# Kernel optimization log

Hardware: AMD Instinct MI355X
Metric: run time of the kernel (lower is better)

The kernel has to match this reference:

```python
import jax, jax.numpy as jnp
import numpy as np


def setup_inputs() -> dict:
    key = jax.random.key(0)
    k_x, k_wxh, k_whh, k_fcw, k_fcb = jax.random.split(key, 5)
    B, T, I, H = 256, 512, 64, 512
    x = jax.random.normal(k_x, (B, T, I), dtype=jnp.float32)
    W_xh = jax.random.normal(k_wxh, (I, H), dtype=jnp.float32) * 0.01
    W_hh = jax.random.normal(k_whh, (H, H), dtype=jnp.float32) * 0.01
    b = jnp.zeros((H,), dtype=jnp.float32)
    # nn.Linear(H, 1): weight (1, H), bias (1); init ~ U(-1/sqrt(H), 1/sqrt(H))
    lim = 1.0 / np.sqrt(H)
    fc_w = jax.random.uniform(k_fcw, (1, H), dtype=jnp.float32, minval=-lim, maxval=lim)
    fc_b = jax.random.uniform(k_fcb, (1,), dtype=jnp.float32, minval=-lim, maxval=lim)
    return {"x": x, "W_xh": W_xh, "W_hh": W_hh, "b": b, "fc_w": fc_w, "fc_b": fc_b}


def reference(x, W_xh, W_hh, b, fc_w, fc_b):
    B, T, I = x.shape
    H = W_hh.shape[0]
    # Precompute input projections for all timesteps in one big matmul: (B,T,H)
    xh = jnp.einsum('bti,ih->bth', x, W_xh) + b
    h0 = jnp.zeros((B, H), dtype=x.dtype)

    def step(h, xh_t):
        h_new = jnp.tanh(xh_t + h @ W_hh)
        return h_new, None

    h_final, _ = jax.lax.scan(step, h0, jnp.swapaxes(xh, 0, 1))  # scan over T
    return h_final @ fc_w.T + fc_b  # (B, 1)
```

## Files before the change

### kernel.cpp

```cpp
#include <hip/hip_runtime.h>


#define BATCH    256
#define TSTEPS   512
#define IDIM     64
#define HDIM     512
#define NTH      512

typedef _Float16 half2_t __attribute__((ext_vector_type(2)));
typedef _Float16 half8_t __attribute__((ext_vector_type(8)));

union H8U {
    half8_t v;
    half2_t p[4];
    uint4   u4;
};

__device__ __forceinline__ float fdot2(half2_t a, half2_t b, float c) {
#if __has_builtin(__builtin_amdgcn_fdot2)
    return __builtin_amdgcn_fdot2(a, b, c, false);
#else
    return c + (float)a[0] * (float)b[0] + (float)a[1] * (float)b[1];
#endif
}

__device__ __forceinline__ float fast_tanh(float x) {
    float e = __builtin_amdgcn_exp2f(x * 2.88539008177792681472f);
    return 1.0f - 2.0f * __builtin_amdgcn_rcpf(e + 1.0f);
}

__device__ __forceinline__ float quad_sum(float x) {
    union { float f; int i; } a, b;
    a.f = x;
    b.i = __builtin_amdgcn_update_dpp(0, a.i, 0xB1, 0xF, 0xF, true);
    a.f += b.f;
    b.i = __builtin_amdgcn_update_dpp(0, a.i, 0x4E, 0xF, 0xF, true);
    a.f += b.f;
    return a.f;
}

#define XH_ROWS 16
__global__ __launch_bounds__(NTH, 4)
void xh_gemm(const float* __restrict__ x, const float* __restrict__ Wxh,
             const float* __restrict__ bias, _Float16* __restrict__ xh)
{
    const int j = threadIdx.x;
    const size_t r0 = (size_t)blockIdx.x * XH_ROWS;
    float wcol[IDIM];
#pragma unroll
    for (int i = 0; i < IDIM; ++i) wcol[i] = Wxh[(size_t)i * HDIM + j];
    const float bj = bias[j];
#pragma unroll
    for (int r = 0; r < XH_ROWS; ++r) {
        const float* xr = x + (r0 + r) * IDIM;
        float acc = bj;
#pragma unroll
        for (int i = 0; i < IDIM; ++i) acc += xr[i] * wcol[i];
        xh[(r0 + r) * HDIM + j] = (_Float16)acc;
    }
}

#define K4_RP      48
#define K4_NW      (4 * K4_RP)
#define K4_STR     17
#define K4_W_BYTES (NTH * K4_STR * 16)
#define K4_HB_OFF   K4_W_BYTES
#define K4_HB_STRIDE 1152
#define K4_RED_OFF  (K4_HB_OFF + 2 * K4_HB_STRIDE)
#define K4_SMEM_BYTES (K4_RED_OFF + 64)

__global__ __attribute__((amdgpu_flat_work_group_size(NTH, NTH), amdgpu_waves_per_eu(2, 2)))
void rnn_k4s(const _Float16* __restrict__ xh,
             const float* __restrict__ Whh,
             const float* __restrict__ fcw,
             const float* __restrict__ fcb,
             float* __restrict__ out)
{
    extern __shared__ char smem[];
    uint4* ldsW = reinterpret_cast<uint4*>(smem);
    float* red  = reinterpret_cast<float*>(smem + K4_RED_OFF);

    const int tid   = threadIdx.x;
    const int q     = tid & 3;
    const int c     = tid >> 2;
    const int j0    = 4 * c;
    const int kbase = 128 * q;
    const int b     = blockIdx.x;

    half2_t wr[K4_NW];
    uint4*  myW = ldsW + tid * K4_STR;
#pragma unroll
    for (int p = 0; p < K4_RP; ++p) {
        const float4 f0 = *reinterpret_cast<const float4*>(Whh + (size_t)(kbase + 2 * p) * HDIM + j0);
        const float4 f1 = *reinterpret_cast<const float4*>(Whh + (size_t)(kbase + 2 * p + 1) * HDIM + j0);
        half2_t w;
        w[0] = (_Float16)f0.x; w[1] = (_Float16)f1.x; wr[4 * p + 0] = w;
        w[0] = (_Float16)f0.y; w[1] = (_Float16)f1.y; wr[4 * p + 1] = w;
        w[0] = (_Float16)f0.z; w[1] = (_Float16)f1.z; wr[4 * p + 2] = w;
        w[0] = (_Float16)f0.w; w[1] = (_Float16)f1.w; wr[4 * p + 3] = w;
    }
#pragma unroll
    for (int cc = 0; cc < 4; ++cc) {
        H8U t0, t1, t2, t3;
#pragma unroll
        for (int e = 0; e < 4; ++e) {
            const int k = kbase + 96 + 8 * cc + 2 * e;
            const float4 f0 = *reinterpret_cast<const float4*>(Whh + (size_t)k * HDIM + j0);
            const float4 f1 = *reinterpret_cast<const float4*>(Whh + (size_t)(k + 1) * HDIM + j0);
            half2_t w;
            w[0] = (_Float16)f0.x; w[1] = (_Float16)f1.x; t0.p[e] = w;
            w[0] = (_Float16)f0.y; w[1] = (_Float16)f1.y; t1.p[e] = w;
            w[0] = (_Float16)f0.z; w[1] = (_Float16)f1.z; t2.p[e] = w;
            w[0] = (_Float16)f0.w; w[1] = (_Float16)f1.w; t3.p[e] = w;
        }
        myW[cc]      = t0.u4;
        myW[4 + cc]  = t1.u4;
        myW[8 + cc]  = t2.u4;
        myW[12 + cc] = t3.u4;
    }

    const char* hb0c = smem + K4_HB_OFF + 288 * q;
    const char* hb1c = hb0c + K4_HB_STRIDE;
    const int   jw   = j0 + q;
    const int   wbyte = 2 * jw + 32 * (jw >> 7);
    _Float16* wp0 = reinterpret_cast<_Float16*>(smem + K4_HB_OFF + wbyte);
    _Float16* wp1 = reinterpret_cast<_Float16*>(smem + K4_HB_OFF + K4_HB_STRIDE + wbyte);

    const float fcwj = fcw[jw];
    const _Float16* xhp = xh + (size_t)b * TSTEPS * HDIM + jw;

    if (tid < 144) {
        uint4 z; z.x = z.y = z.z = z.w = 0u;
        reinterpret_cast<uint4*>(smem + K4_HB_OFF)[tid] = z;
    }
    __syncthreads();

    float hlast = 0.f;
#pragma unroll 1
    for (int t = 0; t < TSTEPS; ++t) {
        const _Float16* hb = reinterpret_cast<const _Float16*>((t & 1) ? hb1c : hb0c);
        const float xv = (float)*xhp;
        xhp += HDIM;

        float a0 = 0.f, b0 = 0.f, a1 = 0.f, b1 = 0.f;
        float a2 = 0.f, b2 = 0.f, a3 = 0.f, b3 = 0.f;
#pragma unroll
        for (int i = 0; i < 12; ++i) {
            H8U u; u.v = *reinterpret_cast<const half8_t*>(hb + 8 * i);
            a0 = fdot2(u.p[0], wr[16*i +  0], a0);
            a1 = fdot2(u.p[0], wr[16*i +  1], a1);
            a2 = fdot2(u.p[0], wr[16*i +  2], a2);
            a3 = fdot2(u.p[0], wr[16*i +  3], a3);
            b0 = fdot2(u.p[1], wr[16*i +  4], b0);
            b1 = fdot2(u.p[1], wr[16*i +  5], b1);
            b2 = fdot2(u.p[1], wr[16*i +  6], b2);
            b3 = fdot2(u.p[1], wr[16*i +  7], b3);
            a0 = fdot2(u.p[2], wr[16*i +  8], a0);
            a1 = fdot2(u.p[2], wr[16*i +  9], a1);
            a2 = fdot2(u.p[2], wr[16*i + 10], a2);
            a3 = fdot2(u.p[2], wr[16*i + 11], a3);
            b0 = fdot2(u.p[3], wr[16*i + 12], b0);
            b1 = fdot2(u.p[3], wr[16*i + 13], b1);
            b2 = fdot2(u.p[3], wr[16*i + 14], b2);
            b3 = fdot2(u.p[3], wr[16*i + 15], b3);
        }
#pragma unroll
        for (int cc = 0; cc < 4; ++cc) {
            H8U u; u.v = *reinterpret_cast<const half8_t*>(hb + 8 * (12 + cc));
            H8U w0; w0.u4 = myW[cc];
            H8U w1; w1.u4 = myW[4 + cc];
            H8U w2; w2.u4 = myW[8 + cc];
            H8U w3; w3.u4 = myW[12 + cc];
            a0 = fdot2(u.p[0], w0.p[0], a0); b0 = fdot2(u.p[1], w0.p[1], b0);
            a0 = fdot2(u.p[2], w0.p[2], a0); b0 = fdot2(u.p[3], w0.p[3], b0);
            a1 = fdot2(u.p[0], w1.p[0], a1); b1 = fdot2(u.p[1], w1.p[1], b1);
            a1 = fdot2(u.p[2], w1.p[2], a1); b1 = fdot2(u.p[3], w1.p[3], b1);
            a2 = fdot2(u.p[0], w2.p[0], a2); b2 = fdot2(u.p[1], w2.p[1], b2);
            a2 = fdot2(u.p[2], w2.p[2], a2); b2 = fdot2(u.p[3], w2.p[3], b2);
            a3 = fdot2(u.p[0], w3.p[0], a3); b3 = fdot2(u.p[1], w3.p[1], b3);
            a3 = fdot2(u.p[2], w3.p[2], a3); b3 = fdot2(u.p[3], w3.p[3], b3);
        }

        const float s0 = quad_sum(a0 + b0);
        const float s1 = quad_sum(a1 + b1);
        const float s2 = quad_sum(a2 + b2);
        const float s3 = quad_sum(a3 + b3);

        const float sq = (q & 2) ? ((q & 1) ? s3 : s2) : ((q & 1) ? s1 : s0);
        const float h  = fast_tanh(sq + xv);
        *((t & 1) ? wp0 : wp1) = (_Float16)h;
        hlast = h;
        __syncthreads();
    }

    float partial = hlast * fcwj;
#pragma unroll
    for (int off = 32; off >= 1; off >>= 1)
        partial += __shfl_down(partial, off, 64);
    if ((tid & 63) == 0) red[tid >> 6] = partial;
    __syncthreads();
    if (tid == 0) {
        float s = 0.f;
#pragma unroll
        for (int w = 0; w < 8; ++w) s += red[w];
        out[b] = s + fcb[0];
    }
}

#define F_RP   216
#define F_RC   54
#define F_LC   18
#define F_LSTR 19
#define F_LDSW_BYTES (512 * F_LSTR * 16)
#define F_HBUF_OFF   F_LDSW_BYTES
#define F_HBUF_ELEMS 640
#define F_RED_OFF    (F_HBUF_OFF + 2 * F_HBUF_ELEMS * 2)
#define F_SMEM_BYTES (F_RED_OFF + 64)

__global__ __attribute__((amdgpu_flat_work_group_size(NTH, NTH), amdgpu_waves_per_eu(2, 2)))
void rnn_fused(const float* __restrict__ x, const float* __restrict__ Wxh,
               const float* __restrict__ Whh, const float* __restrict__ bias,
               const float* __restrict__ fcw, const float* __restrict__ fcb,
               float* __restrict__ out)
{
    extern __shared__ char smem[];
    uint4*    ldsW = reinterpret_cast<uint4*>(smem);
    _Float16* hbuf = reinterpret_cast<_Float16*>(smem + F_HBUF_OFF);
    float*    red  = reinterpret_cast<float*>(smem + F_RED_OFF);

    const int j = threadIdx.x;
    const int b = blockIdx.x;

    half2_t wreg[F_RP];
#pragma unroll
    for (int p = 0; p < F_RP; ++p) {
        const int k = 2 * p;
        half2_t w;
        w[0] = (_Float16)Whh[(size_t)k * HDIM + j];
        w[1] = (_Float16)Whh[(size_t)(k + 1) * HDIM + j];
        wreg[p] = w;
    }
#pragma unroll
    for (int cc = 0; cc < F_LC; ++cc) {
        H8U u;
#pragma unroll
        for (int qq = 0; qq < 4; ++qq) {
            const int k0 = 432 + 8 * cc + 2 * qq;
            const int k1 = k0 + 1;
            half2_t w;
            w[0] = (_Float16)(k0 < HDIM ? Whh[(size_t)k0 * HDIM + j]
                                        : Wxh[(size_t)(k0 - HDIM) * HDIM + j]);
            w[1] = (_Float16)(k1 < HDIM ? Whh[(size_t)k1 * HDIM + j]
                                        : Wxh[(size_t)(k1 - HDIM) * HDIM + j]);
            u.p[qq] = w;
        }
        ldsW[j * F_LSTR + cc] = u.u4;
    }

    const float bj   = bias[j];
    const float fcwj = fcw[j];

    hbuf[j] = (_Float16)0.0f;
    if (j < IDIM) hbuf[HDIM + j] = (_Float16)x[((size_t)b * TSTEPS + 0) * IDIM + j];
    __syncthreads();

    float hval = 0.0f;
    for (int t = 0; t < TSTEPS; ++t) {
        const int cur = t & 1;
        const int nxt = cur ^ 1;
        const _Float16* hb = hbuf + cur * F_HBUF_ELEMS;

        float xv = 0.0f;
        const bool do_x = (j < IDIM) && (t + 1 < TSTEPS);
        if (do_x) xv = x[((size_t)b * TSTEPS + (t + 1)) * IDIM + j];

        float a0 = bj, a1 = 0.0f, a2 = 0.0f, a3 = 0.0f;
#pragma unroll
        for (int c = 0; c < F_RC; ++c) {
            H8U u;
            u.v = *reinterpret_cast<const half8_t*>(hb + 8 * c);
            a0 = fdot2(u.p[0], wreg[4 * c + 0], a0);
            a1 = fdot2(u.p[1], wreg[4 * c + 1], a1);
            a2 = fdot2(u.p[2], wreg[4 * c + 2], a2);
            a3 = fdot2(u.p[3], wreg[4 * c + 3], a3);
        }
#pragma unroll
        for (int cc = 0; cc < F_LC; ++cc) {
            H8U u, w;
            u.v  = *reinterpret_cast<const half8_t*>(hb + 8 * (F_RC + cc));
            w.u4 = ldsW[j * F_LSTR + cc];
            a0 = fdot2(u.p[0], w.p[0], a0);
            a1 = fdot2(u.p[1], w.p[1], a1);
            a2 = fdot2(u.p[2], w.p[2], a2);
            a3 = fdot2(u.p[3], w.p[3], a3);
        }
        hval = fast_tanh((a0 + a1) + (a2 + a3));

        hbuf[nxt * F_HBUF_ELEMS + j] = (_Float16)hval;
        if (do_x) hbuf[nxt * F_HBUF_ELEMS + HDIM + j] = (_Float16)xv;
        __syncthreads();
    }

    float partial = hval * fcwj;
#pragma unroll
    for (int off = 32; off >= 1; off >>= 1)
        partial += __shfl_down(partial, off, 64);
    if ((j & 63) == 0) red[j >> 6] = partial;
    __syncthreads();
    if (j == 0) {
        float s = 0.0f;
#pragma unroll
        for (int w = 0; w < 8; ++w) s += red[w];
        out[b] = s + fcb[0];
    }
}

extern "C" void kernel_launch(void* const* d_in, const int* in_sizes, int n_in,
                              void* d_out, int out_size, void* d_ws, size_t ws_size,
                              hipStream_t stream) {
    const float* x    = (const float*)d_in[0];
    const float* Wxh  = (const float*)d_in[1];
    const float* Whh  = (const float*)d_in[2];
    const float* bias = (const float*)d_in[3];
    const float* fcw  = (const float*)d_in[4];
    const float* fcb  = (const float*)d_in[5];
    float* out = (float*)d_out;

    const size_t xh_bytes = (size_t)BATCH * TSTEPS * HDIM * sizeof(_Float16);
    if (ws_size >= xh_bytes) {
        hipFuncSetAttribute(reinterpret_cast<const void*>(rnn_k4s),
                            hipFuncAttributeMaxDynamicSharedMemorySize, K4_SMEM_BYTES);
        _Float16* xh = (_Float16*)d_ws;
        xh_gemm<<<(BATCH * TSTEPS) / XH_ROWS, NTH, 0, stream>>>(x, Wxh, bias, xh);
        rnn_k4s<<<BATCH, NTH, K4_SMEM_BYTES, stream>>>(xh, Whh, fcw, fcb, out);
    } else {
        hipFuncSetAttribute(reinterpret_cast<const void*>(rnn_fused),
                            hipFuncAttributeMaxDynamicSharedMemorySize, F_SMEM_BYTES);
        rnn_fused<<<BATCH, NTH, F_SMEM_BYTES, stream>>>(x, Wxh, Whh, bias, fcw, fcb, out);
    }
}
```

Baseline: 1.248 ms.

## Batch 16 sequences per block and compute recurrence with MFMA

Adds a new recurrent kernel in which each block handles 16 batch rows and computes h@W_hh with 16x16x32 f16 MFMA instructions. A prep kernel repacks W_hh into an MFMA-friendly f16 layout, and the weight fragments are streamed from global memory (L2) every step instead of being held in registers or LDS. Batching raises arithmetic intensity and uses the matrix cores instead of per-thread dot products, but only 16 blocks are launched, which leaves most CUs idle and makes each step depend on L2 weight bandwidth. The path runs only when the workspace holds both xh and the repacked weights.

After: 2.589 ms. 2.08x slower.

```diff
diff --git a/kernel.cpp b/kernel.cpp
--- a/kernel.cpp
+++ b/kernel.cpp
@@ -7,8 +7,9 @@
 #define HDIM     512
 #define NTH      512
 
-typedef _Float16 half2_t __attribute__((ext_vector_type(2)));
-typedef _Float16 half8_t __attribute__((ext_vector_type(8)));
+typedef _Float16 half2_t  __attribute__((ext_vector_type(2)));
+typedef _Float16 half8_t  __attribute__((ext_vector_type(8)));
+typedef float    f32x4    __attribute__((ext_vector_type(4)));
 
 union H8U {
     half8_t v;
@@ -28,6 +29,144 @@
     float e = __builtin_amdgcn_exp2f(x * 2.88539008177792681472f);
     return 1.0f - 2.0f * __builtin_amdgcn_rcpf(e + 1.0f);
 }
+
+#define XH_ROWS 16
+__global__ __launch_bounds__(NTH, 4)
+void xh_gemm(const float* __restrict__ x, const float* __restrict__ Wxh,
+             const float* __restrict__ bias, _Float16* __restrict__ xh)
+{
+    const int j = threadIdx.x;
+    const size_t r0 = (size_t)blockIdx.x * XH_ROWS;
+    float wcol[IDIM];
+#pragma unroll
+    for (int i = 0; i < IDIM; ++i) wcol[i] = Wxh[(size_t)i * HDIM + j];
+    const float bj = bias[j];
+#pragma unroll
+    for (int r = 0; r < XH_ROWS; ++r) {
+        const float* xr = x + (r0 + r) * IDIM;
+        float acc = bj;
+#pragma unroll
+        for (int i = 0; i < IDIM; ++i) acc += xr[i] * wcol[i];
+        xh[(r0 + r) * HDIM + j] = (_Float16)acc;
+    }
+}
+
+#define KT    16
+#define NJT   32
+__global__ __launch_bounds__(NTH)
+void wt_prep(const float* __restrict__ Whh, _Float16* __restrict__ wt)
+{
+    const int id = blockIdx.x * NTH + threadIdx.x;
+    const int l  = id & 63;
+    const int kt = (id >> 6) & 15;
+    const int jt = id >> 10;
+    const int n     = 16 * jt + (l & 15);
+    const int kbase = 32 * kt + 8 * (l >> 4);
+    _Float16 v[8];
+#pragma unroll
+    for (int e = 0; e < 8; ++e)
+        v[e] = (_Float16)Whh[(size_t)(kbase + e) * HDIM + n];
+    *reinterpret_cast<uint4*>(wt + (size_t)id * 8) = *reinterpret_cast<const uint4*>(v);
+}
+
+#define MPB   16
+#define NBLK  (BATCH / MPB)
+#define HS    536
+
+__global__ __attribute__((amdgpu_flat_work_group_size(NTH, NTH), amdgpu_waves_per_eu(2, 2)))
+void rnn_mfma(const _Float16* __restrict__ xh,
+              const _Float16* __restrict__ wt,
+              const float* __restrict__ fcw,
+              const float* __restrict__ fcb,
+              float* __restrict__ out)
+{
+    __shared__ _Float16 hbuf[2][MPB][HS];
+
+    const int tid  = threadIdx.x;
+    const int l    = tid & 63;
+    const int w    = tid >> 6;
+    const int b0   = blockIdx.x * MPB;
+
+    const int row_c = l & 15;
+    const int kgrp  = l >> 4;
+    const int erow0 = 4 * kgrp;
+
+    for (int i = tid; i < MPB * HS; i += NTH) hbuf[0][0][i] = (_Float16)0.0f;
+
+    int cols[4];
+    const half8_t* wb[4];
+#pragma unroll
+    for (int i = 0; i < 4; ++i) {
+        const int jt = 4 * w + i;
+        cols[i] = 16 * jt + row_c;
+        wb[i]   = reinterpret_cast<const half8_t*>(wt + ((size_t)jt * KT * 64 + l) * 8);
+    }
+    const _Float16* xrow[4];
+#pragma unroll
+    for (int r = 0; r < 4; ++r)
+        xrow[r] = xh + (size_t)(b0 + erow0 + r) * TSTEPS * HDIM;
+
+    __syncthreads();
+
+#pragma unroll 1
+    for (int t = 0; t < TSTEPS; ++t) {
+        const _Float16 (*hb)[HS] = hbuf[t & 1];
+        _Float16 (*hn)[HS]       = hbuf[(t & 1) ^ 1];
+
+        float xv[4][4];
+        const size_t toff = (size_t)t * HDIM;
+#pragma unroll
+        for (int i = 0; i < 4; ++i)
+#pragma unroll
+            for (int r = 0; r < 4; ++r)
+                xv[i][r] = (float)xrow[r][toff + cols[i]];
+
+        f32x4 acc0 = {0.f, 0.f, 0.f, 0.f};
+        f32x4 acc1 = {0.f, 0.f, 0.f, 0.f};
+        f32x4 acc2 = {0.f, 0.f, 0.f, 0.f};
+        f32x4 acc3 = {0.f, 0.f, 0.f, 0.f};
+
+#pragma unroll
+        for (int kt = 0; kt < KT; ++kt) {
+            const half8_t a = *reinterpret_cast<const half8_t*>(
+                &hb[row_c][32 * kt + 8 * kgrp]);
+            const half8_t bf0 = wb[0][(size_t)kt * 64];
+            const half8_t bf1 = wb[1][(size_t)kt * 64];
+            const half8_t bf2 = wb[2][(size_t)kt * 64];
+            const half8_t bf3 = wb[3][(size_t)kt * 64];
+            acc0 = __builtin_amdgcn_mfma_f32_16x16x32_f16(a, bf0, acc0, 0, 0, 0);
+            acc1 = __builtin_amdgcn_mfma_f32_16x16x32_f16(a, bf1, acc1, 0, 0, 0);
+            acc2 = __builtin_amdgcn_mfma_f32_16x16x32_f16(a, bf2, acc2, 0, 0, 0);
+            acc3 = __builtin_amdgcn_mfma_f32_16x16x32_f16(a, bf3, acc3, 0, 0, 0);
+        }
+
+#pragma unroll
+        for (int r = 0; r < 4; ++r) {
+            hn[erow0 + r][cols[0]] = (_Float16)fast_tanh(acc0[r] + xv[0][r]);
+            hn[erow0 + r][cols[1]] = (_Float16)fast_tanh(acc1[r] + xv[1][r]);
+            hn[erow0 + r][cols[2]] = (_Float16)fast_tanh(acc2[r] + xv[2][r]);
+            hn[erow0 + r][cols[3]] = (_Float16)fast_tanh(acc3[r] + xv[3][r]);
+        }
+        __syncthreads();
+    }
+
+    const int m = tid >> 5;
+    const int s = tid & 31;
+    float p = 0.f;
+    for (int j = s; j < HDIM; j += 32) p += (float)hbuf[0][m][j] * fcw[j];
+#pragma unroll
+    for (int off = 16; off >= 1; off >>= 1) p += __shfl_down(p, off, 32);
+    if (s == 0) out[b0 + m] = p + fcb[0];
+}
+
+#define K4_RP      48
+#define K4_NW      (4 * K4_RP)
+#define K4_STR     17
+#define K4_W_BYTES (NTH * K4_STR * 16)
+#define K4_HB_OFF   K4_W_BYTES
+#define K4_HB_STRIDE 1152
+#define K4_RED_OFF  (K4_HB_OFF + 2 * K4_HB_STRIDE)
+#define K4_SMEM_BYTES (K4_RED_OFF + 64)
 
 __device__ __forceinline__ float quad_sum(float x) {
     union { float f; int i; } a, b;
@@ -39,41 +178,9 @@
     return a.f;
 }
 
-#define XH_ROWS 16
-__global__ __launch_bounds__(NTH, 4)
-void xh_gemm(const float* __restrict__ x, const float* __restrict__ Wxh,
-             const float* __restrict__ bias, _Float16* __restrict__ xh)
-{
-    const int j = threadIdx.x;
-    const size_t r0 = (size_t)blockIdx.x * XH_ROWS;
-    float wcol[IDIM];
-#pragma unroll
-    for (int i = 0; i < IDIM; ++i) wcol[i] = Wxh[(size_t)i * HDIM + j];
-    const float bj = bias[j];
-#pragma unroll
-    for (int r = 0; r < XH_ROWS; ++r) {
-        const float* xr = x + (r0 + r) * IDIM;
-        float acc = bj;
-#pragma unroll
-        for (int i = 0; i < IDIM; ++i) acc += xr[i] * wcol[i];
-        xh[(r0 + r) * HDIM + j] = (_Float16)acc;
-    }
-}
-
-#define K4_RP      48
-#define K4_NW      (4 * K4_RP)
-#define K4_STR     17
-#define K4_W_BYTES (NTH * K4_STR * 16)
-#define K4_HB_OFF   K4_W_BYTES
-#define K4_HB_STRIDE 1152
-#define K4_RED_OFF  (K4_HB_OFF + 2 * K4_HB_STRIDE)
-#define K4_SMEM_BYTES (K4_RED_OFF + 64)
-
 __global__ __attribute__((amdgpu_flat_work_group_size(NTH, NTH), amdgpu_waves_per_eu(2, 2)))
-void rnn_k4s(const _Float16* __restrict__ xh,
-             const float* __restrict__ Whh,
-             const float* __restrict__ fcw,
-             const float* __restrict__ fcb,
+void rnn_k4s(const _Float16* __restrict__ xh, const float* __restrict__ Whh,
+             const float* __restrict__ fcw, const float* __restrict__ fcb,
              float* __restrict__ out)
 {
     extern __shared__ char smem[];
@@ -113,15 +220,12 @@
             w[0] = (_Float16)f0.z; w[1] = (_Float16)f1.z; t2.p[e] = w;
             w[0] = (_Float16)f0.w; w[1] = (_Float16)f1.w; t3.p[e] = w;
         }
-        myW[cc]      = t0.u4;
-        myW[4 + cc]  = t1.u4;
-        myW[8 + cc]  = t2.u4;
-        myW[12 + cc] = t3.u4;
+        myW[cc] = t0.u4; myW[4 + cc] = t1.u4; myW[8 + cc] = t2.u4; myW[12 + cc] = t3.u4;
     }
 
     const char* hb0c = smem + K4_HB_OFF + 288 * q;
     const char* hb1c = hb0c + K4_HB_STRIDE;
-    const int   jw   = j0 + q;
+    const int   jw    = j0 + q;
     const int   wbyte = 2 * jw + 32 * (jw >> 7);
     _Float16* wp0 = reinterpret_cast<_Float16*>(smem + K4_HB_OFF + wbyte);
     _Float16* wp1 = reinterpret_cast<_Float16*>(smem + K4_HB_OFF + K4_HB_STRIDE + wbyte);
@@ -202,7 +306,7 @@
     if (tid == 0) {
         float s = 0.f;
 #pragma unroll
-        for (int w = 0; w < 8; ++w) s += red[w];
+        for (int w2 = 0; w2 < 8; ++w2) s += red[w2];
         out[b] = s + fcb[0];
     }
 }
@@ -310,7 +414,7 @@
     if (j == 0) {
         float s = 0.0f;
 #pragma unroll
-        for (int w = 0; w < 8; ++w) s += red[w];
+        for (int w2 = 0; w2 < 8; ++w2) s += red[w2];
         out[b] = s + fcb[0];
     }
 }
@@ -327,7 +431,15 @@
     float* out = (float*)d_out;
 
     const size_t xh_bytes = (size_t)BATCH * TSTEPS * HDIM * sizeof(_Float16);
-    if (ws_size >= xh_bytes) {
+    const size_t wt_bytes = (size_t)HDIM * HDIM * sizeof(_Float16);
+
+    if (ws_size >= xh_bytes + wt_bytes) {
+        _Float16* xh = (_Float16*)d_ws;
+        _Float16* wt = (_Float16*)((char*)d_ws + xh_bytes);
+        wt_prep<<<(NJT * KT * 64) / NTH, NTH, 0, stream>>>(Whh, wt);
+        xh_gemm<<<(BATCH * TSTEPS) / XH_ROWS, NTH, 0, stream>>>(x, Wxh, bias, xh);
+        rnn_mfma<<<NBLK, NTH, 0, stream>>>(xh, wt, fcw, fcb, out);
+    } else if (ws_size >= xh_bytes) {
         hipFuncSetAttribute(reinterpret_cast<const void*>(rnn_k4s),
                             hipFuncAttributeMaxDynamicSharedMemorySize, K4_SMEM_BYTES);
         _Float16* xh = (_Float16*)d_ws;
```
